# Optimization experiments

Measured on AMD Instinct MI355X. Metric: run time of the kernel, lower is better.

## Reference

```python
import jax, jax.numpy as jnp
import numpy as np

N, XC, YC, H, W_ = 1024, 512, 256, 8, 8
HID = 512


def setup_inputs() -> dict:
    key = jax.random.key(0)
    k = jax.random.split(key, 6)
    x_samples = jax.random.normal(k[0], (N, XC, H, W_), dtype=jnp.float32)
    y_samples = jax.random.normal(k[1], (N, YC, H, W_), dtype=jnp.float32)
    # p_mu: Linear(x_dim, hidden) -> ReLU -> Linear(hidden, y_dim)
    s1 = 1.0 / np.sqrt(XC)
    s2 = 1.0 / np.sqrt(HID)
    W1 = jax.random.uniform(k[2], (XC, HID), jnp.float32, -s1, s1)
    b1 = jax.random.uniform(k[3], (HID,), jnp.float32, -s1, s1)
    W2 = jax.random.uniform(k[4], (HID, YC), jnp.float32, -s2, s2)
    b2 = jax.random.uniform(k[5], (YC,), jnp.float32, -s2, s2)
    return {"x_samples": x_samples, "y_samples": y_samples,
            "W1": W1, "b1": b1, "W2": W2, "b2": b2}


def reference(x_samples, y_samples, W1, b1, W2, b2):
    # AdaptiveAvgPool2d(1) + flatten(1) == mean over spatial dims
    x_vec = x_samples.mean(axis=(2, 3))  # (N, x_dim)
    y_vec = y_samples.mean(axis=(2, 3))  # (N, y_dim)
    # p_mu MLP
    h = jax.nn.relu(x_vec @ W1 + b1)
    mu = h @ W2 + b2  # (N, y_dim)
    # positive: -(mu_i - y_i)^2 / 2, summed over D
    positive = (-((mu - y_vec) ** 2) / 2.0).sum(axis=-1)  # (N,)
    # negative: for each i, mean_j (y_j - mu_i)^2 / 2, summed over D
    diff = y_vec[None, :, :] - mu[:, None, :]  # (N, N, D)
    negative = (-(diff ** 2).mean(axis=1) / 2.0).sum(axis=-1)  # (N,)
    return (positive - negative).mean()
```

## Files before the change

### kernel.cpp

```cpp
#include <hip/hip_runtime.h>

#define N_SAMP 1024
#define XC_DIM 512
#define YC_DIM 256
#define HID_DIM 512

__global__ __launch_bounds__(256, 2) void pool_kernel(
    const float* __restrict__ x, const float* __restrict__ y,
    float* __restrict__ x_vec, float* __restrict__ y_vec) {
  __shared__ float s[256 * 17];
  const int t = threadIdx.x;
  const long blk = blockIdx.x;
  const float4* src;
  float* dst;
  long obase;
  if (blk < 2048) {
    src = (const float4*)x; dst = x_vec; obase = blk * 256;
  } else {
    src = (const float4*)y; dst = y_vec; obase = (blk - 2048) * 256;
  }
  const float4* p = src + obase * 16;

  float4 v[16];
#pragma unroll
  for (int k = 0; k < 16; ++k) v[k] = p[k * 256 + t];

#pragma unroll
  for (int k = 0; k < 16; ++k) {
    float sv = (v[k].x + v[k].y) + (v[k].z + v[k].w);
    const int o = k * 16 + (t >> 4);
    const int j = t & 15;
    s[o * 17 + j] = sv;
  }
  __syncthreads();
  float acc = 0.f;
#pragma unroll
  for (int j = 0; j < 16; ++j) acc += s[t * 17 + j];
  dst[obase + t] = acc * (1.0f / 64.0f);
}

#define TBK 16

__global__ __launch_bounds__(256) void gemm1_kernel(
    const float* __restrict__ A, const float* __restrict__ B,
    float* __restrict__ Hp) {
  const int K = 512, Nn = 512;
  __shared__ float As[TBK][68];
  __shared__ float Bs[TBK][68];
  const int t = threadIdx.x;
  const int bn = blockIdx.x * 64;
  const int bm = blockIdx.y * 64;
  const int ks = blockIdx.z;

  const int arow = t >> 2, acol = (t & 3) * 4;
  const int brow = t >> 4, bcol = (t & 15) * 4;
  const int row0 = (t >> 4) * 4, col0 = (t & 15) * 4;

  float acc[4][4] = {};
  const int k0 = ks * 128;

  float4 av = *(const float4*)&A[(bm + arow) * K + k0 + acol];
  float4 bv = *(const float4*)&B[(k0 + brow) * Nn + bn + bcol];

  for (int it = 0; it < 8; ++it) {
    __syncthreads();
    As[acol + 0][arow] = av.x;
    As[acol + 1][arow] = av.y;
    As[acol + 2][arow] = av.z;
    As[acol + 3][arow] = av.w;
    *(float4*)&Bs[brow][bcol] = bv;
    __syncthreads();
    if (it < 7) {
      const int k1 = k0 + (it + 1) * TBK;
      av = *(const float4*)&A[(bm + arow) * K + k1 + acol];
      bv = *(const float4*)&B[(k1 + brow) * Nn + bn + bcol];
    }
#pragma unroll
    for (int kk = 0; kk < TBK; ++kk) {
      float4 a = *(const float4*)&As[kk][row0];
      float4 b = *(const float4*)&Bs[kk][col0];
      acc[0][0] += a.x * b.x; acc[0][1] += a.x * b.y; acc[0][2] += a.x * b.z; acc[0][3] += a.x * b.w;
      acc[1][0] += a.y * b.x; acc[1][1] += a.y * b.y; acc[1][2] += a.y * b.z; acc[1][3] += a.y * b.w;
      acc[2][0] += a.z * b.x; acc[2][1] += a.z * b.y; acc[2][2] += a.z * b.z; acc[2][3] += a.z * b.w;
      acc[3][0] += a.w * b.x; acc[3][1] += a.w * b.y; acc[3][2] += a.w * b.z; acc[3][3] += a.w * b.w;
    }
  }

  float* H = Hp + (long)ks * (N_SAMP * HID_DIM);
#pragma unroll
  for (int i = 0; i < 4; ++i) {
    float4 o;
    o.x = acc[i][0]; o.y = acc[i][1]; o.z = acc[i][2]; o.w = acc[i][3];
    *(float4*)&H[(long)(bm + row0 + i) * Nn + bn + col0] = o;
  }
}

__global__ __launch_bounds__(256) void gemm2_kernel(
    const float* __restrict__ Hp, const float* __restrict__ b1,
    const float* __restrict__ B, float* __restrict__ Mup) {
  const int K = 512, Nn = 256;
  __shared__ float As[TBK][68];
  __shared__ float Bs[TBK][68];
  const int t = threadIdx.x;
  const int bn = blockIdx.x * 64;
  const int bm = blockIdx.y * 64;
  const int ks = blockIdx.z;
  const long HS = (long)N_SAMP * HID_DIM;

  const int arow = t >> 2, acol = (t & 3) * 4;
  const int brow = t >> 4, bcol = (t & 15) * 4;
  const int row0 = (t >> 4) * 4, col0 = (t & 15) * 4;

  float acc[4][4] = {};
  const int k0 = ks * 64;

  long aidx = (long)(bm + arow) * K + k0 + acol;
  float4 a0 = *(const float4*)&Hp[aidx];
  float4 a1 = *(const float4*)&Hp[aidx + HS];
  float4 a2 = *(const float4*)&Hp[aidx + 2 * HS];
  float4 a3 = *(const float4*)&Hp[aidx + 3 * HS];
  float4 bb = *(const float4*)&b1[k0 + acol];
  float4 bv = *(const float4*)&B[(k0 + brow) * Nn + bn + bcol];

  for (int it = 0; it < 4; ++it) {
    float4 av;
    av.x = fmaxf(a0.x + a1.x + a2.x + a3.x + bb.x, 0.0f);
    av.y = fmaxf(a0.y + a1.y + a2.y + a3.y + bb.y, 0.0f);
    av.z = fmaxf(a0.z + a1.z + a2.z + a3.z + bb.z, 0.0f);
    av.w = fmaxf(a0.w + a1.w + a2.w + a3.w + bb.w, 0.0f);
    __syncthreads();
    As[acol + 0][arow] = av.x;
    As[acol + 1][arow] = av.y;
    As[acol + 2][arow] = av.z;
    As[acol + 3][arow] = av.w;
    *(float4*)&Bs[brow][bcol] = bv;
    __syncthreads();
    if (it < 3) {
      const int k1 = k0 + (it + 1) * TBK;
      aidx = (long)(bm + arow) * K + k1 + acol;
      a0 = *(const float4*)&Hp[aidx];
      a1 = *(const float4*)&Hp[aidx + HS];
      a2 = *(const float4*)&Hp[aidx + 2 * HS];
      a3 = *(const float4*)&Hp[aidx + 3 * HS];
      bb = *(const float4*)&b1[k1 + acol];
      bv = *(const float4*)&B[(k1 + brow) * Nn + bn + bcol];
    }
#pragma unroll
    for (int kk = 0; kk < TBK; ++kk) {
      float4 a = *(const float4*)&As[kk][row0];
      float4 b = *(const float4*)&Bs[kk][col0];
      acc[0][0] += a.x * b.x; acc[0][1] += a.x * b.y; acc[0][2] += a.x * b.z; acc[0][3] += a.x * b.w;
      acc[1][0] += a.y * b.x; acc[1][1] += a.y * b.y; acc[1][2] += a.y * b.z; acc[1][3] += a.y * b.w;
      acc[2][0] += a.z * b.x; acc[2][1] += a.z * b.y; acc[2][2] += a.z * b.z; acc[2][3] += a.z * b.w;
      acc[3][0] += a.w * b.x; acc[3][1] += a.w * b.y; acc[3][2] += a.w * b.z; acc[3][3] += a.w * b.w;
    }
  }

  float* M = Mup + (long)ks * (N_SAMP * YC_DIM);
#pragma unroll
  for (int i = 0; i < 4; ++i) {
    float4 o;
    o.x = acc[i][0]; o.y = acc[i][1]; o.z = acc[i][2]; o.w = acc[i][3];
    *(float4*)&M[(long)(bm + row0 + i) * Nn + bn + col0] = o;
  }
}

__global__ __launch_bounds__(256) void reduce_kernel(
    const float* __restrict__ Mup, const float* __restrict__ b2,
    const float* __restrict__ yv, float* __restrict__ colsum_mu,
    float* __restrict__ colsum_y, float* __restrict__ dot_out) {
  const int d = threadIdx.x;
  const int n0 = blockIdx.x * 16;
  const long MS = (long)N_SAMP * YC_DIM;
  const float bb = b2[d];
  float cm = 0.f, cy = 0.f, dp = 0.f;
#pragma unroll 4
  for (int r = 0; r < 16; ++r) {
    const long idx = (long)(n0 + r) * YC_DIM + d;
    float mu = bb;
#pragma unroll
    for (int s = 0; s < 8; ++s) mu += Mup[idx + s * MS];
    const float yy = yv[idx];
    dp += mu * yy;
    cm += mu;
    cy += yy;
  }
  atomicAdd(&colsum_mu[d], cm);
  atomicAdd(&colsum_y[d], cy);
#pragma unroll
  for (int off = 1; off < 64; off <<= 1) dp += __shfl_xor(dp, off);
  if ((d & 63) == 0) atomicAdd(dot_out, dp);
}

__global__ __launch_bounds__(256) void finalize_kernel(
    const float* __restrict__ colsum_mu, const float* __restrict__ colsum_y,
    const float* __restrict__ dot_in, float* __restrict__ out) {
  __shared__ float partial[4];
  const int t = threadIdx.x;
  float v = colsum_mu[t] * colsum_y[t];
#pragma unroll
  for (int off = 1; off < 64; off <<= 1) v += __shfl_xor(v, off);
  if ((t & 63) == 0) partial[t >> 6] = v;
  __syncthreads();
  if (t == 0) {
    float tot = partial[0] + partial[1] + partial[2] + partial[3];
    out[0] = dot_in[0] * (1.0f / 1024.0f) - tot * (1.0f / (1024.0f * 1024.0f));
  }
}

extern "C" void kernel_launch(void* const* d_in, const int* in_sizes, int n_in,
                              void* d_out, int out_size, void* d_ws, size_t ws_size,
                              hipStream_t stream) {
  const float* x  = (const float*)d_in[0];
  const float* y  = (const float*)d_in[1];
  const float* W1 = (const float*)d_in[2];
  const float* b1 = (const float*)d_in[3];
  const float* W2 = (const float*)d_in[4];
  const float* b2 = (const float*)d_in[5];
  float* out = (float*)d_out;

  char* ws = (char*)d_ws;
  float* x_vec = (float*)ws;
  float* y_vec = (float*)(ws + (2lu << 20));
  float* Hp    = (float*)(ws + (4lu << 20));
  float* Mup   = (float*)(ws + (12lu << 20));
  float* accum = (float*)(ws + (20lu << 20));
  float* colsum_mu = accum;
  float* colsum_y  = accum + 256;
  float* dotp      = accum + 512;

  hipMemsetAsync(accum, 0, 513 * sizeof(float), stream);

  pool_kernel<<<3072, 256, 0, stream>>>(x, y, x_vec, y_vec);

  gemm1_kernel<<<dim3(8, 16, 4), 256, 0, stream>>>(x_vec, W1, Hp);

  gemm2_kernel<<<dim3(4, 16, 8), 256, 0, stream>>>(Hp, b1, W2, Mup);

  reduce_kernel<<<64, 256, 0, stream>>>(Mup, b2, y_vec, colsum_mu,
                                        colsum_y, dotp);

  finalize_kernel<<<1, 256, 0, stream>>>(colsum_mu, colsum_y, dotp, out);
}
```

Baseline: 275.6 us.

## Fuse reduction into gemm2 epilogue and use nontemporal loads in pooling

```diff
diff --git a/kernel.cpp b/kernel.cpp
--- a/kernel.cpp
+++ b/kernel.cpp
@@ -5,25 +5,28 @@
 #define YC_DIM 256
 #define HID_DIM 512
 
+typedef float float4n __attribute__((ext_vector_type(4)));
+
 __global__ __launch_bounds__(256, 2) void pool_kernel(
     const float* __restrict__ x, const float* __restrict__ y,
     float* __restrict__ x_vec, float* __restrict__ y_vec) {
   __shared__ float s[256 * 17];
   const int t = threadIdx.x;
   const long blk = blockIdx.x;
-  const float4* src;
+  const float4n* src;
   float* dst;
   long obase;
   if (blk < 2048) {
-    src = (const float4*)x; dst = x_vec; obase = blk * 256;
+    src = (const float4n*)x; dst = x_vec; obase = blk * 256;
   } else {
-    src = (const float4*)y; dst = y_vec; obase = (blk - 2048) * 256;
-  }
-  const float4* p = src + obase * 16;
-
-  float4 v[16];
-#pragma unroll
-  for (int k = 0; k < 16; ++k) v[k] = p[k * 256 + t];
+    src = (const float4n*)y; dst = y_vec; obase = (blk - 2048) * 256;
+  }
+  const float4n* p = src + obase * 16;
+
+  float4n v[16];
+#pragma unroll
+  for (int k = 0; k < 16; ++k) v[k] = __builtin_nontemporal_load(&p[k * 256 + t]);
+  __builtin_amdgcn_sched_barrier(0);
 
 #pragma unroll
   for (int k = 0; k < 16; ++k) {
@@ -97,10 +100,14 @@
 
 __global__ __launch_bounds__(256) void gemm2_kernel(
     const float* __restrict__ Hp, const float* __restrict__ b1,
-    const float* __restrict__ B, float* __restrict__ Mup) {
+    const float* __restrict__ B, const float* __restrict__ yvec,
+    float* __restrict__ colsum_mu, float* __restrict__ colsum_y,
+    float* __restrict__ dot_out) {
   const int K = 512, Nn = 256;
   __shared__ float As[TBK][68];
   __shared__ float Bs[TBK][68];
+  __shared__ float s_cm[64];
+  __shared__ float s_cy[64];
   const int t = threadIdx.x;
   const int bn = blockIdx.x * 64;
   const int bm = blockIdx.y * 64;
@@ -110,6 +117,8 @@
   const int arow = t >> 2, acol = (t & 3) * 4;
   const int brow = t >> 4, bcol = (t & 15) * 4;
   const int row0 = (t >> 4) * 4, col0 = (t & 15) * 4;
+
+  if (t < 64) { s_cm[t] = 0.f; s_cy[t] = 0.f; }
 
   float acc[4][4] = {};
   const int k0 = ks * 64;
@@ -156,55 +165,54 @@
     }
   }
 
-  float* M = Mup + (long)ks * (N_SAMP * YC_DIM);
+  float dp = 0.f;
+  float cm[4] = {};
+  float cy[4] = {};
 #pragma unroll
   for (int i = 0; i < 4; ++i) {
-    float4 o;
-    o.x = acc[i][0]; o.y = acc[i][1]; o.z = acc[i][2]; o.w = acc[i][3];
-    *(float4*)&M[(long)(bm + row0 + i) * Nn + bn + col0] = o;
-  }
-}
-
-__global__ __launch_bounds__(256) void reduce_kernel(
-    const float* __restrict__ Mup, const float* __restrict__ b2,
-    const float* __restrict__ yv, float* __restrict__ colsum_mu,
-    float* __restrict__ colsum_y, float* __restrict__ dot_out) {
-  const int d = threadIdx.x;
-  const int n0 = blockIdx.x * 16;
-  const long MS = (long)N_SAMP * YC_DIM;
-  const float bb = b2[d];
-  float cm = 0.f, cy = 0.f, dp = 0.f;
-#pragma unroll 4
-  for (int r = 0; r < 16; ++r) {
-    const long idx = (long)(n0 + r) * YC_DIM + d;
-    float mu = bb;
-#pragma unroll
-    for (int s = 0; s < 8; ++s) mu += Mup[idx + s * MS];
-    const float yy = yv[idx];
-    dp += mu * yy;
-    cm += mu;
-    cy += yy;
-  }
-  atomicAdd(&colsum_mu[d], cm);
-  atomicAdd(&colsum_y[d], cy);
+    float4 yv4 = *(const float4*)&yvec[(long)(bm + row0 + i) * Nn + bn + col0];
+    dp += acc[i][0] * yv4.x + acc[i][1] * yv4.y + acc[i][2] * yv4.z + acc[i][3] * yv4.w;
+    cm[0] += acc[i][0]; cm[1] += acc[i][1]; cm[2] += acc[i][2]; cm[3] += acc[i][3];
+    cy[0] += yv4.x; cy[1] += yv4.y; cy[2] += yv4.z; cy[3] += yv4.w;
+  }
+  __syncthreads();
+#pragma unroll
+  for (int c = 0; c < 4; ++c) atomicAdd(&s_cm[col0 + c], cm[c]);
+  if (ks == 0) {
+#pragma unroll
+    for (int c = 0; c < 4; ++c) atomicAdd(&s_cy[col0 + c], cy[c]);
+  }
 #pragma unroll
   for (int off = 1; off < 64; off <<= 1) dp += __shfl_xor(dp, off);
-  if ((d & 63) == 0) atomicAdd(dot_out, dp);
+  if ((t & 63) == 0) atomicAdd(dot_out, dp);
+  __syncthreads();
+  if (t < 64) {
+    atomicAdd(&colsum_mu[bn + t], s_cm[t]);
+    if (ks == 0) atomicAdd(&colsum_y[bn + t], s_cy[t]);
+  }
 }
 
 __global__ __launch_bounds__(256) void finalize_kernel(
     const float* __restrict__ colsum_mu, const float* __restrict__ colsum_y,
-    const float* __restrict__ dot_in, float* __restrict__ out) {
-  __shared__ float partial[4];
-  const int t = threadIdx.x;
-  float v = colsum_mu[t] * colsum_y[t];
-#pragma unroll
-  for (int off = 1; off < 64; off <<= 1) v += __shfl_xor(v, off);
-  if ((t & 63) == 0) partial[t >> 6] = v;
+    const float* __restrict__ b2, const float* __restrict__ dot_in,
+    float* __restrict__ out) {
+  __shared__ float p1[4], p2[4];
+  const int t = threadIdx.x;
+  const float cy = colsum_y[t];
+  const float bb = b2[t];
+  float v1 = bb * cy;
+  float v2 = cy * (colsum_mu[t] + 1024.0f * bb);
+#pragma unroll
+  for (int off = 1; off < 64; off <<= 1) {
+    v1 += __shfl_xor(v1, off);
+    v2 += __shfl_xor(v2, off);
+  }
+  if ((t & 63) == 0) { p1[t >> 6] = v1; p2[t >> 6] = v2; }
   __syncthreads();
   if (t == 0) {
-    float tot = partial[0] + partial[1] + partial[2] + partial[3];
-    out[0] = dot_in[0] * (1.0f / 1024.0f) - tot * (1.0f / (1024.0f * 1024.0f));
+    float s1 = p1[0] + p1[1] + p1[2] + p1[3];
+    float s2 = p2[0] + p2[1] + p2[2] + p2[3];
+    out[0] = (dot_in[0] + s1) * (1.0f / 1024.0f) - s2 * (1.0f / (1024.0f * 1024.0f));
   }
 }
 
@@ -223,22 +231,19 @@
   float* x_vec = (float*)ws;
   float* y_vec = (float*)(ws + (2lu << 20));
   float* Hp    = (float*)(ws + (4lu << 20));
-  float* Mup   = (float*)(ws + (12lu << 20));
-  float* accum = (float*)(ws + (20lu << 20));
+  float* accum = (float*)(ws + (12lu << 20));
   float* colsum_mu = accum;
   float* colsum_y  = accum + 256;
   float* dotp      = accum + 512;
 
-  hipMemsetAsync(accum, 0, 513 * sizeof(float), stream);
+  (void)hipMemsetAsync(accum, 0, 513 * sizeof(float), stream);
 
   pool_kernel<<<3072, 256, 0, stream>>>(x, y, x_vec, y_vec);
 
   gemm1_kernel<<<dim3(8, 16, 4), 256, 0, stream>>>(x_vec, W1, Hp);
 
-  gemm2_kernel<<<dim3(4, 16, 8), 256, 0, stream>>>(Hp, b1, W2, Mup);
-
-  reduce_kernel<<<64, 256, 0, stream>>>(Mup, b2, y_vec, colsum_mu,
-                                        colsum_y, dotp);
-
-  finalize_kernel<<<1, 256, 0, stream>>>(colsum_mu, colsum_y, dotp, out);
-}
+  gemm2_kernel<<<dim3(4, 16, 8), 256, 0, stream>>>(Hp, b1, W2, y_vec,
+                                                   colsum_mu, colsum_y, dotp);
+
+  finalize_kernel<<<1, 256, 0, stream>>>(colsum_mu, colsum_y, b2, dotp, out);
+}
```

Result: no change. 275.8 us (+0.1%).
